# Kernel tuning notes

Measured on AMD Instinct MI355X. Metric: run time of the kernel, lower is better.

## Reference

```python
import jax, jax.numpy as jnp
import numpy as np

EMBED = 1024
HEADS = 16
GQA_GROUPS = 2
KV_HEADS = HEADS // GQA_GROUPS  # 8
HEAD_DIM = EMBED // HEADS       # 64
ALIBI_ALPHA = 1.0
START_I = 0
N, S = 2, 2048


def setup_inputs() -> dict:
    key = jax.random.key(0)
    ks = jax.random.split(key, 6)
    x = jax.random.normal(ks[0], (N, S, EMBED), dtype=jnp.float32)
    sc = 1.0 / np.sqrt(EMBED)
    Wq = jax.random.normal(ks[1], (HEADS * HEAD_DIM, EMBED), dtype=jnp.float32) * sc
    Wk = jax.random.normal(ks[2], (KV_HEADS * HEAD_DIM, EMBED), dtype=jnp.float32) * sc
    Wv = jax.random.normal(ks[3], (KV_HEADS * HEAD_DIM, EMBED), dtype=jnp.float32) * sc
    Wo = jax.random.normal(ks[4], (EMBED, HEADS * HEAD_DIM), dtype=jnp.float32) * sc
    bo = jax.random.normal(ks[5], (EMBED,), dtype=jnp.float32) * 0.01
    return {"x": x, "Wq": Wq, "Wk": Wk, "Wv": Wv, "Wo": Wo, "bo": bo}


def _alibi_bias(q_len, k_len):
    # slopes[i] = 2**(-alpha*(i+start)) for i in 1..heads  -> shape (1,H,1,1)
    i = jnp.arange(1, HEADS + 1, dtype=jnp.float32)
    slopes = jnp.exp2(-ALIBI_ALPHA * (i + START_I)).reshape(1, HEADS, 1, 1)
    t_q = jnp.arange(q_len, dtype=jnp.float32)
    t_k = jnp.arange(k_len, dtype=jnp.float32)
    dist = jnp.abs(t_q[:, None] - t_k[None, :])  # (Q,K), symmetric (non-causal ALiBi)
    return -dist[None, None] * slopes            # (1,H,Q,K)


def reference(x, Wq, Wk, Wv, Wo, bo):
    n, s, _ = x.shape
    q = (x @ Wq.T).reshape(n, s, HEADS, HEAD_DIM)      # nqhd
    k = (x @ Wk.T).reshape(n, s, KV_HEADS, HEAD_DIM)   # nkhd (kv heads)
    v = (x @ Wv.T).reshape(n, s, KV_HEADS, HEAD_DIM)
    # GQA: repeat_interleave kv heads along head dim
    k = jnp.repeat(k, GQA_GROUPS, axis=2)
    v = jnp.repeat(v, GQA_GROUPS, axis=2)
    energy = jnp.einsum("nqhd,nkhd->nhqk", q, k)
    energy = energy + _alibi_bias(s, s)
    # NOTE: original divides (energy + bias) by sqrt(head_dim) inside softmax
    attn = jax.nn.softmax(energy / jnp.sqrt(jnp.float32(HEAD_DIM)), axis=-1)
    out = jnp.einsum("nhqk,nkhd->nqhd", attn, v).reshape(n, s, HEADS * HEAD_DIM)
    return out @ Wo.T + bo
```

## Files before the change

kernel.cpp:

```cpp
#include <hip/hip_runtime.h>

typedef _Float16 f16;
typedef f16 f16x8 __attribute__((ext_vector_type(8)));
typedef f16 f16x4 __attribute__((ext_vector_type(4)));
typedef float f32x4 __attribute__((ext_vector_type(4)));
typedef float f32x16 __attribute__((ext_vector_type(16)));
typedef unsigned uint4v __attribute__((ext_vector_type(4)));

#define GLL(g, l) __builtin_amdgcn_global_load_lds((const __attribute__((address_space(1))) void*)(g), (__attribute__((address_space(3))) void*)(l), 16, 0, 0)

__global__ __launch_bounds__(256) void cvt_all(
    const float* __restrict__ x, const float* __restrict__ wq, const float* __restrict__ wk,
    const float* __restrict__ wv, const float* __restrict__ wo,
    f16* __restrict__ xh, f16* __restrict__ wqh, f16* __restrict__ wkh,
    f16* __restrict__ wvh, f16* __restrict__ woh)
{
  int i = blockIdx.x * 256 + threadIdx.x;
  const float4* src; f16x4* dst; int off;
  if (i < 1048576)      { src = (const float4*)x;  dst = (f16x4*)xh;  off = i; }
  else if (i < 1310720) { src = (const float4*)wq; dst = (f16x4*)wqh; off = i - 1048576; }
  else if (i < 1441792) { src = (const float4*)wk; dst = (f16x4*)wkh; off = i - 1310720; }
  else if (i < 1572864) { src = (const float4*)wv; dst = (f16x4*)wvh; off = i - 1441792; }
  else                  { src = (const float4*)wo; dst = (f16x4*)woh; off = i - 1572864; }
  float4 v = src[off];
  f16x4 hv; hv[0] = (f16)v.x; hv[1] = (f16)v.y; hv[2] = (f16)v.z; hv[3] = (f16)v.w;
  dst[off] = hv;
}

template<int MODE>
__global__ __launch_bounds__(256) void gemm_k(
    const f16* __restrict__ A, const f16* __restrict__ B0, const f16* __restrict__ B1,
    f16* __restrict__ Qb, f16* __restrict__ Kb,
    const float* __restrict__ bo, float* __restrict__ Co)
{
  __shared__ __align__(16) f16 Ah[2][4096];
  __shared__ __align__(16) f16 Bh[2][4096];
  const int tid = threadIdx.x;
  const int bm = blockIdx.x & 31, bn = blockIdx.x >> 5;
  const f16* Bp;
  if (MODE == 0) {
    if (bn < 8)  Bp = B0 + (size_t)bn * 131072;
    else         Bp = B1 + (size_t)(bn - 8) * 131072;
  } else {
    Bp = B0 + (size_t)bn * 131072;
  }
  const f16* Ap = A + (size_t)bm * 131072;

  const int w = tid >> 6, lane = tid & 63, lr = lane & 15, lg = lane >> 4;
  const int wr = w >> 1, wc = w & 1;

  auto stage = [&](int b, int kt) {
#pragma unroll
    for (int i = 0; i < 2; ++i) {
      int o = tid * 16 + i * 4096;
      int row = o >> 6, colb = o & 63;
      GLL((const char*)Ap + (size_t)row * 2048 + kt * 64 + colb, (char*)&Ah[b][0] + o);
      GLL((const char*)Bp + (size_t)row * 2048 + kt * 64 + colb, (char*)&Bh[b][0] + o);
    }
  };

  f32x4 acc[4][4] = {};

  stage(0, 0);
  for (int kt = 0; kt < 32; ++kt) {
    const int cur = kt & 1;
    __syncthreads();
    if (kt < 31) stage(cur ^ 1, kt + 1);
    f16x8 af[4], bf[4];
#pragma unroll
    for (int mi = 0; mi < 4; ++mi)
      af[mi] = *(const f16x8*)((const char*)&Ah[cur][0] + (wr * 64 + mi * 16 + lr) * 64 + lg * 16);
#pragma unroll
    for (int ni = 0; ni < 4; ++ni)
      bf[ni] = *(const f16x8*)((const char*)&Bh[cur][0] + (wc * 64 + ni * 16 + lr) * 64 + lg * 16);
#pragma unroll
    for (int mi = 0; mi < 4; ++mi)
#pragma unroll
      for (int ni = 0; ni < 4; ++ni)
        acc[mi][ni] = __builtin_amdgcn_mfma_f32_16x16x32_f16(af[mi], bf[ni], acc[mi][ni], 0, 0, 0);
    __syncthreads();
  }

  const float C1 = 0.18033688011112042f;
#pragma unroll
  for (int mi = 0; mi < 4; ++mi) {
#pragma unroll
    for (int ni = 0; ni < 4; ++ni) {
      const int ncol = bn * 128 + wc * 64 + ni * 16 + lr;
#pragma unroll
      for (int j = 0; j < 4; ++j) {
        const int m = bm * 128 + wr * 64 + mi * 16 + lg * 4 + j;
        const float v = acc[mi][ni][j];
        if (MODE == 0) {
          const int nb = m >> 11, s = m & 2047;
          if (ncol < 1024) {
            const int hh = ncol >> 6, d = ncol & 63;
            Qb[(((size_t)(nb * 16 + hh)) * 2048 + s) * 64 + d] = (f16)(v * C1);
          } else {
            const int kh = (ncol - 1024) >> 6, d = ncol & 63;
            const int tb2 = s >> 6, rr = s & 63;
            const int kt2 = rr >> 5, lq2 = rr & 31;
            const int cd2 = d >> 4, hi2 = (d >> 3) & 1, e2 = d & 7;
            Kb[((((size_t)(nb * 8 + kh) * 32 + tb2) * 8 + kt2 * 4 + cd2) * 64 + hi2 * 32 + lq2) * 8 + e2] = (f16)v;
          }
        } else {
          Co[(size_t)m * 1024 + ncol] = v + bo[ncol];
        }
      }
    }
  }
}

__global__ __launch_bounds__(256) void gemm_vt(
    const f16* __restrict__ A,
    const f16* __restrict__ B,
    f16* __restrict__ C)
{
  __shared__ __align__(16) f16 Ah[2][2048];
  __shared__ __align__(16) f16 Bh[2][4096];
  const int tid = threadIdx.x;
  const int bm = blockIdx.x & 7, bn = blockIdx.x >> 3;
  const f16* Ap = A + (size_t)bm * 65536;
  const f16* Bp = B + (size_t)bn * 131072;
  const int w = tid >> 6, lane = tid & 63, lr = lane & 15, lg = lane >> 4;
  const int wr = w >> 1, wc = w & 1;

  auto stage = [&](int b, int kt) {
    {
      int o = tid * 16;
      int row = o >> 6, colb = o & 63;
      GLL((const char*)Ap + (size_t)row * 2048 + kt * 64 + colb, (char*)&Ah[b][0] + o);
    }
#pragma unroll
    for (int i = 0; i < 2; ++i) {
      int o = tid * 16 + i * 4096;
      int row = o >> 6, colb = o & 63;
      GLL((const char*)Bp + (size_t)row * 2048 + kt * 64 + colb, (char*)&Bh[b][0] + o);
    }
  };

  f32x4 acc[2][4] = {};
  stage(0, 0);
  for (int kt = 0; kt < 32; ++kt) {
    const int cur = kt & 1;
    __syncthreads();
    if (kt < 31) stage(cur ^ 1, kt + 1);
    f16x8 af[2], bf[4];
#pragma unroll
    for (int mi = 0; mi < 2; ++mi)
      af[mi] = *(const f16x8*)((const char*)&Ah[cur][0] + (wr * 32 + mi * 16 + lr) * 64 + lg * 16);
#pragma unroll
    for (int ni = 0; ni < 4; ++ni)
      bf[ni] = *(const f16x8*)((const char*)&Bh[cur][0] + (wc * 64 + ni * 16 + lr) * 64 + lg * 16);
#pragma unroll
    for (int mi = 0; mi < 2; ++mi)
#pragma unroll
      for (int ni = 0; ni < 4; ++ni)
        acc[mi][ni] = __builtin_amdgcn_mfma_f32_16x16x32_f16(af[mi], bf[ni], acc[mi][ni], 0, 0, 0);
    __syncthreads();
  }

#pragma unroll
  for (int mi = 0; mi < 2; ++mi)
#pragma unroll
    for (int ni = 0; ni < 4; ++ni) {
      const int ncol = bn * 128 + wc * 64 + ni * 16 + lr;
      const int nn = ncol >> 11, s = ncol & 2047;
      const int tb2 = s >> 6, kk = s & 63;
      const int ck2 = kk >> 4, hi2 = (kk >> 3) & 1, e2 = kk & 7;
#pragma unroll
      for (int j = 0; j < 4; ++j) {
        const int m = bm * 64 + wr * 32 + mi * 16 + lg * 4 + j;
        const int kvh2 = m >> 6, d = m & 63;
        const int dt2 = d >> 5, lq2 = d & 31;
        C[((((size_t)(nn * 8 + kvh2) * 32 + tb2) * 8 + dt2 * 4 + ck2) * 64 + hi2 * 32 + lq2) * 8 + e2] = (f16)acc[mi][ni][j];
      }
    }
}

__global__ __launch_bounds__(256, 4) void attn_k(
    const f16* __restrict__ Qb, const f16* __restrict__ Kf, const f16* __restrict__ Vf,
    f16* __restrict__ Ob)
{
  __shared__ __align__(16) char SMEM[26112];

  const int tid = threadIdx.x, w = tid >> 6, l = tid & 63;
  const int lq = l & 31, hi = l >> 5;
  const int qt = blockIdx.x, nh = blockIdx.y;
  const int n = nh >> 4, h = nh & 15, kvh = h >> 1;
  const int qb = qt * 32;
  const int qhat = qb + lq;

  const f16* Qp = Qb + ((size_t)(n * 16 + h) * 2048 + qhat) * 64;
  f16x8 qf[4];
#pragma unroll
  for (int cd = 0; cd < 4; ++cd)
    qf[cd] = *(const f16x8*)(Qp + cd * 16 + hi * 8);

  const f16* Klane = Kf + (size_t)(n * 8 + kvh) * 131072 + l * 8;
  const f16* Vlane = Vf + (size_t)(n * 8 + kvh) * 131072 + l * 8;

  f32x16 oacc[2] = {};
  f32x16 lacc = {};
  float m_r = -1e30f;
  const float C1 = 0.18033688011112042f;
  const float slt = exp2f(-(float)(h + 1)) * C1;
  const float qpos = (float)qhat;

  f16x8 ones;
#pragma unroll
  for (int i = 0; i < 8; ++i) ones[i] = (f16)1.0f;

  for (int t = 0; t < 8; ++t) {
    const int tb = w * 8 + t;
    const f16* Kt_ = Klane + (size_t)tb * 4096;
    const f16* Vt_ = Vlane + (size_t)tb * 4096;

#pragma unroll
    for (int kt = 0; kt < 2; ++kt) {
      f32x16 c = {};
#pragma unroll
      for (int cd = 0; cd < 4; ++cd) {
        f16x8 kf = *(const f16x8*)(Kt_ + (kt * 4 + cd) * 512);
        c = __builtin_amdgcn_mfma_f32_32x32x16_f16(kf, qf[cd], c, 0, 0, 0);
      }
      const float kb0 = (float)(tb * 64 + kt * 32 + 4 * hi);
      float p[16];
#pragma unroll
      for (int r = 0; r < 16; ++r) {
        float kpos = kb0 + (float)((r & 3) + 8 * (r >> 2));
        p[r] = fmaf(-fabsf(qpos - kpos), slt, c[r]);
      }
      float mx[8];
#pragma unroll
      for (int r = 0; r < 8; ++r) mx[r] = fmaxf(p[r], p[r + 8]);
#pragma unroll
      for (int st = 4; st; st >>= 1)
#pragma unroll
        for (int r = 0; r < st; ++r) mx[r] = fmaxf(mx[r], mx[r + st]);
      float pmax = fmaxf(mx[0], __shfl_xor(mx[0], 32));
      if (!__all(pmax - m_r <= 8.0f)) {
        float mn = fmaxf(m_r, pmax);
        float sc = __builtin_amdgcn_exp2f(m_r - mn);
        m_r = mn;
#pragma unroll
        for (int dt = 0; dt < 2; ++dt)
#pragma unroll
          for (int r = 0; r < 16; ++r) oacc[dt][r] *= sc;
#pragma unroll
        for (int r = 0; r < 16; ++r) lacc[r] *= sc;
      }
#pragma unroll
      for (int r = 0; r < 16; ++r)
        p[r] = __builtin_amdgcn_exp2f(p[r] - m_r);

      f16x8 pfv[2];
#pragma unroll
      for (int e = 0; e < 2; ++e) {
        unsigned w0 = __builtin_bit_cast(unsigned, __builtin_amdgcn_cvt_pkrtz(p[8 * e + 0], p[8 * e + 1]));
        unsigned w2 = __builtin_bit_cast(unsigned, __builtin_amdgcn_cvt_pkrtz(p[8 * e + 4], p[8 * e + 5]));
        unsigned w1 = __builtin_bit_cast(unsigned, __builtin_amdgcn_cvt_pkrtz(p[8 * e + 2], p[8 * e + 3]));
        unsigned w3 = __builtin_bit_cast(unsigned, __builtin_amdgcn_cvt_pkrtz(p[8 * e + 6], p[8 * e + 7]));
        asm volatile("v_permlane32_swap_b32 %0, %1" : "+v"(w0), "+v"(w2));
        asm volatile("v_permlane32_swap_b32 %0, %1" : "+v"(w1), "+v"(w3));
        uint4v pu; pu.x = w0; pu.y = w1; pu.z = w2; pu.w = w3;
        pfv[e] = __builtin_bit_cast(f16x8, pu);
      }

#pragma unroll
      for (int dt = 0; dt < 2; ++dt) {
#pragma unroll
        for (int e = 0; e < 2; ++e) {
          f16x8 vfr = *(const f16x8*)(Vt_ + (dt * 4 + kt * 2 + e) * 512);
          oacc[dt] = __builtin_amdgcn_mfma_f32_32x32x16_f16(vfr, pfv[e], oacc[dt], 0, 0, 0);
        }
      }
      lacc = __builtin_amdgcn_mfma_f32_32x32x16_f16(ones, pfv[0], lacc, 0, 0, 0);
      lacc = __builtin_amdgcn_mfma_f32_32x32x16_f16(ones, pfv[1], lacc, 0, 0, 0);
    }
  }

  float l_r = lacc[0];

  float* Xo = (float*)SMEM;
  float* Xm = (float*)(SMEM + 25344);
  float* Xl = (float*)(SMEM + 25728);
  f16* Ot = (f16*)SMEM;

  __syncthreads();
  if (w) {
    const int set = w - 1;
#pragma unroll
    for (int dt = 0; dt < 2; ++dt)
#pragma unroll
      for (int r = 0; r < 16; ++r) {
        const int d = dt * 32 + (r & 3) + 8 * (r >> 2) + 4 * hi;
        Xo[(set * 32 + lq) * 66 + d] = oacc[dt][r];
      }
    if (!hi) { Xm[set * 32 + lq] = m_r; Xl[set * 32 + lq] = l_r; }
  }
  __syncthreads();
  if (!w) {
#pragma unroll
    for (int set = 0; set < 3; ++set) {
      const float m1 = Xm[set * 32 + lq], l1 = Xl[set * 32 + lq];
      const float mm = fmaxf(m_r, m1);
      const float a0 = __builtin_amdgcn_exp2f(m_r - mm);
      const float a1 = __builtin_amdgcn_exp2f(m1 - mm);
      m_r = mm; l_r = l_r * a0 + l1 * a1;
#pragma unroll
      for (int dt = 0; dt < 2; ++dt)
#pragma unroll
        for (int r = 0; r < 16; ++r) {
          const int d = dt * 32 + (r & 3) + 8 * (r >> 2) + 4 * hi;
          oacc[dt][r] = oacc[dt][r] * a0 + Xo[(set * 32 + lq) * 66 + d] * a1;
        }
    }
  }
  __syncthreads();
  if (!w) {
    const float linv = 1.0f / l_r;
#pragma unroll
    for (int dt = 0; dt < 2; ++dt)
#pragma unroll
      for (int r = 0; r < 16; ++r) {
        const int d = dt * 32 + (r & 3) + 8 * (r >> 2) + 4 * hi;
        Ot[lq * 72 + d] = (f16)(oacc[dt][r] * linv);
      }
  }
  __syncthreads();
  {
    const int q = tid >> 3, seg = tid & 7;
    const f16* src = &Ot[q * 72 + seg * 8];
    f16* dst = Ob + (size_t)(n * 2048 + qb + q) * 1024 + h * 64 + seg * 8;
    *(f16x8*)(dst) = *(const f16x8*)(src);
  }
}

extern "C" void kernel_launch(void* const* d_in, const int* in_sizes, int n_in,
                              void* d_out, int out_size, void* d_ws, size_t ws_size,
                              hipStream_t stream) {
  const float* x  = (const float*)d_in[0];
  const float* Wq = (const float*)d_in[1];
  const float* Wk = (const float*)d_in[2];
  const float* Wv = (const float*)d_in[3];
  const float* Wo = (const float*)d_in[4];
  const float* bo = (const float*)d_in[5];

  char* ws = (char*)d_ws;
  f16* xh  = (f16*)(ws);
  f16* wqh = (f16*)(ws + 8388608);
  f16* wkh = (f16*)(ws + 10485760);
  f16* wvh = (f16*)(ws + 11534336);
  f16* woh = (f16*)(ws + 12582912);
  f16* Qb  = (f16*)(ws + 14680064);
  f16* Kb  = (f16*)(ws + 23068672);
  f16* VTb = (f16*)(ws + 27262976);
  f16* Ob  = (f16*)(ws + 31457280);

  cvt_all<<<7168, 256, 0, stream>>>(x, Wq, Wk, Wv, Wo, xh, wqh, wkh, wvh, woh);
  gemm_k<0><<<384, 256, 0, stream>>>(xh, wqh, wkh, Qb, Kb, nullptr, nullptr);
  gemm_vt<<<256, 256, 0, stream>>>(wvh, xh, VTb);
  attn_k<<<dim3(64, 32), 256, 0, stream>>>(Qb, Kb, VTb, Ob);
  gemm_k<1><<<256, 256, 0, stream>>>(Ob, woh, nullptr, nullptr, nullptr, bo, (float*)d_out);
}
```

Before: 157.7 us.

## Restructure attention blocks to 128 queries with two-way key split per block

The attention kernel now uses 512-thread blocks covering 128 query rows. Four wave groups each take 32 queries, and the key range is split into two halves of 16 tiles each, instead of four waves splitting keys for 32 queries. This lets waves in a block share K/V cache lines across more queries and simplifies the cross-wave softmax merge to a single two-way combine with fewer barriers. In exchange there are fewer blocks, a serial key loop twice as long per wave, and more shared memory per block.

```diff
diff --git a/kernel.cpp b/kernel.cpp
--- a/kernel.cpp
+++ b/kernel.cpp
@@ -178,18 +178,19 @@
     }
 }
 
-__global__ __launch_bounds__(256, 4) void attn_k(
+__global__ __launch_bounds__(512, 2) void attn_k(
     const f16* __restrict__ Qb, const f16* __restrict__ Kf, const f16* __restrict__ Vf,
     f16* __restrict__ Ob)
 {
-  __shared__ __align__(16) char SMEM[26112];
+  __shared__ __align__(16) char SMEM[34816];
 
   const int tid = threadIdx.x, w = tid >> 6, l = tid & 63;
   const int lq = l & 31, hi = l >> 5;
+  const int qg = w & 3, half = w >> 2;
   const int qt = blockIdx.x, nh = blockIdx.y;
   const int n = nh >> 4, h = nh & 15, kvh = h >> 1;
-  const int qb = qt * 32;
-  const int qhat = qb + lq;
+  const int qb = qt * 128;
+  const int qhat = qb + qg * 32 + lq;
 
   const f16* Qp = Qb + ((size_t)(n * 16 + h) * 2048 + qhat) * 64;
   f16x8 qf[4];
@@ -211,8 +212,8 @@
 #pragma unroll
   for (int i = 0; i < 8; ++i) ones[i] = (f16)1.0f;
 
-  for (int t = 0; t < 8; ++t) {
-    const int tb = w * 8 + t;
+  for (int t = 0; t < 16; ++t) {
+    const int tb = half * 16 + t;
     const f16* Kt_ = Klane + (size_t)tb * 4096;
     const f16* Vt_ = Vlane + (size_t)tb * 4096;
 
@@ -283,57 +284,54 @@
   float l_r = lacc[0];
 
   float* Xo = (float*)SMEM;
-  float* Xm = (float*)(SMEM + 25344);
-  float* Xl = (float*)(SMEM + 25728);
+  float* Xl = (float*)(SMEM + 33792);
+  float* Xm = (float*)(SMEM + 34304);
   f16* Ot = (f16*)SMEM;
-
-  __syncthreads();
-  if (w) {
-    const int set = w - 1;
+  const int base = qg * 32 + lq;
+
+  if (half) {
 #pragma unroll
     for (int dt = 0; dt < 2; ++dt)
 #pragma unroll
       for (int r = 0; r < 16; ++r) {
         const int d = dt * 32 + (r & 3) + 8 * (r >> 2) + 4 * hi;
-        Xo[(set * 32 + lq) * 66 + d] = oacc[dt][r];
-      }
-    if (!hi) { Xm[set * 32 + lq] = m_r; Xl[set * 32 + lq] = l_r; }
+        Xo[(size_t)base * 66 + d] = oacc[dt][r];
+      }
+    if (!hi) { Xl[base] = l_r; Xm[base] = m_r; }
   }
   __syncthreads();
-  if (!w) {
-#pragma unroll
-    for (int set = 0; set < 3; ++set) {
-      const float m1 = Xm[set * 32 + lq], l1 = Xl[set * 32 + lq];
-      const float mm = fmaxf(m_r, m1);
-      const float a0 = __builtin_amdgcn_exp2f(m_r - mm);
-      const float a1 = __builtin_amdgcn_exp2f(m1 - mm);
-      m_r = mm; l_r = l_r * a0 + l1 * a1;
-#pragma unroll
-      for (int dt = 0; dt < 2; ++dt)
-#pragma unroll
-        for (int r = 0; r < 16; ++r) {
-          const int d = dt * 32 + (r & 3) + 8 * (r >> 2) + 4 * hi;
-          oacc[dt][r] = oacc[dt][r] * a0 + Xo[(set * 32 + lq) * 66 + d] * a1;
-        }
-    }
-  }
-  __syncthreads();
-  if (!w) {
-    const float linv = 1.0f / l_r;
+  float fin[2][16];
+  if (!half) {
+    const float m1 = Xm[base], l1 = Xl[base];
+    const float mm = fmaxf(m_r, m1);
+    const float a0 = __builtin_amdgcn_exp2f(m_r - mm);
+    const float a1 = __builtin_amdgcn_exp2f(m1 - mm);
+    const float linv = 1.0f / (l_r * a0 + l1 * a1);
 #pragma unroll
     for (int dt = 0; dt < 2; ++dt)
 #pragma unroll
       for (int r = 0; r < 16; ++r) {
         const int d = dt * 32 + (r & 3) + 8 * (r >> 2) + 4 * hi;
-        Ot[lq * 72 + d] = (f16)(oacc[dt][r] * linv);
+        fin[dt][r] = (oacc[dt][r] * a0 + Xo[(size_t)base * 66 + d] * a1) * linv;
+      }
+  }
+  __syncthreads();
+  if (!half) {
+#pragma unroll
+    for (int dt = 0; dt < 2; ++dt)
+#pragma unroll
+      for (int r = 0; r < 16; ++r) {
+        const int d = dt * 32 + (r & 3) + 8 * (r >> 2) + 4 * hi;
+        Ot[base * 72 + d] = (f16)fin[dt][r];
       }
   }
   __syncthreads();
   {
-    const int q = tid >> 3, seg = tid & 7;
-    const f16* src = &Ot[q * 72 + seg * 8];
-    f16* dst = Ob + (size_t)(n * 2048 + qb + q) * 1024 + h * 64 + seg * 8;
+    const int q = tid >> 2, seg = tid & 3;
+    const f16* src = &Ot[q * 72 + seg * 16];
+    f16* dst = Ob + (size_t)(n * 2048 + qb + q) * 1024 + h * 64 + seg * 16;
     *(f16x8*)(dst) = *(const f16x8*)(src);
+    *(f16x8*)(dst + 8) = *(const f16x8*)(src + 8);
   }
 }
 
@@ -361,6 +359,6 @@
   cvt_all<<<7168, 256, 0, stream>>>(x, Wq, Wk, Wv, Wo, xh, wqh, wkh, wvh, woh);
   gemm_k<0><<<384, 256, 0, stream>>>(xh, wqh, wkh, Qb, Kb, nullptr, nullptr);
   gemm_vt<<<256, 256, 0, stream>>>(wvh, xh, VTb);
-  attn_k<<<dim3(64, 32), 256, 0, stream>>>(Qb, Kb, VTb, Ob);
+  attn_k<<<dim3(16, 32), 512, 0, stream>>>(Qb, Kb, VTb, Ob);
   gemm_k<1><<<256, 256, 0, stream>>>(Ob, woh, nullptr, nullptr, nullptr, bo, (float*)d_out);
 }
```

Result: slower. 163.0 us (+3.4%).
